# Kernel optimization log

Measured on AMD Instinct MI355X. Metric: run time of the kernel, lower is better.

The kernel has to match this reference:

```python
import jax, jax.numpy as jnp
import numpy as np

N_EMBD = 768
N_HEAD = 12
HEAD_DIM = N_EMBD // N_HEAD


def setup_inputs() -> dict:
    key = jax.random.key(0)
    ks = jax.random.split(key, 5)
    B, S = 4, 2048
    x = jax.random.normal(ks[0], (B, S, N_EMBD), dtype=jnp.float32)
    scale = 0.02
    w_attn = jax.random.normal(ks[1], (N_EMBD, 3 * N_EMBD), dtype=jnp.float32) * scale
    b_attn = jnp.zeros((3 * N_EMBD,), dtype=jnp.float32)
    w_proj = jax.random.normal(ks[2], (N_EMBD, N_EMBD), dtype=jnp.float32) * scale
    b_proj = jnp.zeros((N_EMBD,), dtype=jnp.float32)
    return {"x": x, "w_attn": w_attn, "b_attn": b_attn, "w_proj": w_proj, "b_proj": b_proj}


def reference(x, w_attn, b_attn, w_proj, b_proj):
    B, S, E = x.shape
    qkv = x @ w_attn + b_attn  # [B,S,3E]
    q, k, v = jnp.split(qkv, 3, axis=2)
    # [B,H,S,D]
    q = q.reshape(B, S, N_HEAD, HEAD_DIM).transpose(0, 2, 1, 3)
    k = k.reshape(B, S, N_HEAD, HEAD_DIM).transpose(0, 2, 1, 3)
    v = v.reshape(B, S, N_HEAD, HEAD_DIM).transpose(0, 2, 1, 3)
    scores = jnp.einsum('bhqd,bhkd->bhqk', q, k) / jnp.sqrt(jnp.float32(HEAD_DIM))
    causal = jnp.tril(jnp.ones((S, S), dtype=bool))
    scores = jnp.where(causal[None, None], scores, jnp.float32(-jnp.inf))
    weights = jax.nn.softmax(scores, axis=-1)
    out = jnp.einsum('bhqk,bhkd->bhqd', weights, v)
    out = out.transpose(0, 2, 1, 3).reshape(B, S, E)
    return out @ w_proj + b_proj
```

## Files before the change

kernel.cpp:

```cpp
#include <hip/hip_runtime.h>
#include <hip/hip_bf16.h>

typedef __attribute__((ext_vector_type(8))) __bf16 bf16x8;
typedef __attribute__((ext_vector_type(4))) __bf16 bf16x4;
typedef __attribute__((ext_vector_type(4))) float f32x4;

#define E_ 768
#define HEADS 12
#define HD 64
#define S_ 2048
#define B_ 4

__device__ inline unsigned short f2bf(float f) {
    union { float f; unsigned int u; } x{f};
    unsigned int r = x.u + 0x7FFFu + ((x.u >> 16) & 1u);
    return (unsigned short)(r >> 16);
}

__global__ void cvt_kernel(const float* __restrict__ in, unsigned short* __restrict__ out, int n4) {
    int i = blockIdx.x * blockDim.x + threadIdx.x;
    if (i < n4) {
        float4 v = reinterpret_cast<const float4*>(in)[i];
        ushort4 o;
        o.x = f2bf(v.x); o.y = f2bf(v.y); o.z = f2bf(v.z); o.w = f2bf(v.w);
        reinterpret_cast<ushort4*>(out)[i] = o;
    }
}

__global__ void transpose_cvt(const float* __restrict__ w, unsigned short* __restrict__ wT,
                              int K, int N) {
    __shared__ float tile[32][33];
    int n0 = blockIdx.x * 32, k0 = blockIdx.y * 32;
    int tx = threadIdx.x, ty = threadIdx.y;
    tile[ty][tx] = w[(size_t)(k0 + ty) * N + n0 + tx];
    __syncthreads();
    wT[(size_t)(n0 + ty) * K + k0 + tx] = f2bf(tile[tx][ty]);
}

template<int MODE>
__global__ __launch_bounds__(256) void gemm16(
    const unsigned short* __restrict__ A, const unsigned short* __restrict__ Bt,
    const float* __restrict__ bias,
    unsigned short* __restrict__ Qo, unsigned short* __restrict__ Ko,
    unsigned short* __restrict__ Vt, float* __restrict__ Of,
    int M, int N, int K)
{
    __shared__ unsigned short Sh[128 * 128];
    unsigned short* Ash = Sh;
    unsigned short* Bsh = Sh + 128 * 64;

    const int nbx = N >> 7;
    const int nwg = (M >> 7) * nbx;
    const int cpx = nwg >> 3;
    const int orig = blockIdx.x;
    const int wgid = (orig & 7) * cpx + (orig >> 3);
    const int row0 = (wgid / nbx) * 128;
    const int col0 = (wgid % nbx) * 128;

    const int t = threadIdx.x;
    const int w = t >> 6, lane = t & 63;
    const int lr = lane & 15, lc = lane >> 4;
    const int wrow = (w >> 1) * 64;
    const int wcol = (w & 1) * 64;

    const int srow = lane >> 3;
    const int sslot = lane & 7;

    f32x4 acc[4][4] = {};

    for (int k0 = 0; k0 < K; k0 += 64) {
#pragma unroll
        for (int j = 0; j < 4; j++) {
            const int rbase = j * 32 + w * 8;
            const unsigned short* ga = A + (size_t)(row0 + rbase + srow) * K + k0 + sslot * 8;
            __builtin_amdgcn_global_load_lds(
                (const __attribute__((address_space(1))) void*)ga,
                (__attribute__((address_space(3))) void*)&Ash[rbase * 64], 16, 0, 0);
            const unsigned short* gb = Bt + (size_t)(col0 + rbase + srow) * K + k0 + sslot * 8;
            __builtin_amdgcn_global_load_lds(
                (const __attribute__((address_space(1))) void*)gb,
                (__attribute__((address_space(3))) void*)&Bsh[rbase * 64], 16, 0, 0);
        }
        __syncthreads();

#pragma unroll
        for (int ks = 0; ks < 2; ks++) {
            bf16x8 a[4], b[4];
#pragma unroll
            for (int i = 0; i < 4; i++)
                a[i] = *reinterpret_cast<const bf16x8*>(&Ash[(wrow + i * 16 + lr) * 64 + ks * 32 + lc * 8]);
#pragma unroll
            for (int j2 = 0; j2 < 4; j2++)
                b[j2] = *reinterpret_cast<const bf16x8*>(&Bsh[(wcol + j2 * 16 + lr) * 64 + ks * 32 + lc * 8]);
#pragma unroll
            for (int i = 0; i < 4; i++)
#pragma unroll
                for (int j2 = 0; j2 < 4; j2++)
                    acc[i][j2] = __builtin_amdgcn_mfma_f32_16x16x32_bf16(a[i], b[j2], acc[i][j2], 0, 0, 0);
        }
        __syncthreads();
    }

    if constexpr (MODE == 0) {
        if (col0 >= 2 * E_) {
#pragma unroll
            for (int i = 0; i < 4; i++)
#pragma unroll
                for (int j = 0; j < 4; j++) {
                    const int c = wcol + j * 16 + lr;
                    const float bv = bias[col0 + c];
#pragma unroll
                    for (int r = 0; r < 4; r++) {
                        const int row = wrow + i * 16 + lc * 4 + r;
                        Sh[c * 128 + (row ^ ((c & 15) << 3))] = f2bf(acc[i][j][r] + bv);
                    }
                }
            __syncthreads();
            const int bb = row0 >> 11;
            const int s0 = row0 & (S_ - 1);
            const int nnb = col0 - 2 * E_;
#pragma unroll
            for (int pass = 0; pass < 8; pass++) {
                const int c = pass * 16 + (t >> 4);
                const int sL = (t & 15) * 8;
                bf16x8 vv = *reinterpret_cast<const bf16x8*>(&Sh[c * 128 + (sL ^ ((c & 15) << 3))]);
                const int h = (nnb + c) >> 6, d = c & 63;
                const size_t bh = (size_t)(bb * HEADS + h);
                *reinterpret_cast<bf16x8*>(&Vt[(bh * HD + d) * S_ + s0 + sL]) = vv;
            }
            return;
        }
#pragma unroll
        for (int i = 0; i < 4; i++)
#pragma unroll
            for (int j = 0; j < 4; j++) {
                int col = col0 + wcol + j * 16 + lr;
                float bv = bias[col];
#pragma unroll
                for (int r = 0; r < 4; r++) {
                    int row = row0 + wrow + i * 16 + lc * 4 + r;
                    float val = acc[i][j][r] + bv;
                    int bb = row >> 11, s = row & (S_ - 1);
                    int which = col / E_;
                    int nn = col - which * E_;
                    int h = nn >> 6, d = nn & 63;
                    size_t bh = (size_t)(bb * HEADS + h);
                    if (which == 0)      Qo[(bh * S_ + s) * HD + d] = f2bf(val * 0.125f);
                    else                 Ko[(bh * S_ + s) * HD + d] = f2bf(val);
                }
            }
    } else {
#pragma unroll
        for (int i = 0; i < 4; i++)
#pragma unroll
            for (int j = 0; j < 4; j++) {
                int col = col0 + wcol + j * 16 + lr;
                float bv = bias[col];
#pragma unroll
                for (int r = 0; r < 4; r++) {
                    int row = row0 + wrow + i * 16 + lc * 4 + r;
                    Of[(size_t)row * N + col] = acc[i][j][r] + bv;
                }
            }
    }
}

__global__ __launch_bounds__(256) void attn_kernel(
    const unsigned short* __restrict__ Q, const unsigned short* __restrict__ Kd,
    const unsigned short* __restrict__ Vt, unsigned short* __restrict__ O)
{
    __shared__ unsigned short Ksh[128 * 64];
    __shared__ unsigned short Vsh[64 * 128];
    __shared__ unsigned short Pl[4][16 * 128];

    const int t = threadIdx.x;
    const int w = t >> 6, lane = t & 63;
    const int lr = lane & 15, lc = lane >> 4;
    const int g = blockIdx.x;
    const int bp = g / 48;
    const int bh = g - bp * 48;
    const int tTL = bp, tTH = 31 - bp;
    const int qLrow0 = tTL * 64 + w * 16;
    const int qHrow0 = tTH * 64 + w * 16;
    const int nL = (tTL + 2) >> 1;

    const unsigned short* Qb = Q + (size_t)bh * S_ * HD;
    const unsigned short* Kb = Kd + (size_t)bh * S_ * HD;
    const unsigned short* Vb = Vt + (size_t)bh * HD * S_;

    const int srK = t >> 3, ssK = t & 7;
    const int kws = ((ssK ^ (srK & 7)) << 3);
    const int srV = t >> 4, ssV = t & 15;
    const int vws = ((ssV ^ (srV & 15)) << 3);
    const int r7 = lr & 7;

    const unsigned short* KbS = Kb + (size_t)srK * HD + ssK * 8;
    const unsigned short* VbS = Vb + (size_t)srV * S_ + ssV * 8;

    bf16x8 aqL[2], aqH[2];
#pragma unroll
    for (int dc = 0; dc < 2; dc++) {
        aqL[dc] = *reinterpret_cast<const bf16x8*>(Qb + (size_t)(qLrow0 + lr) * HD + dc * 32 + lc * 8);
        aqH[dc] = *reinterpret_cast<const bf16x8*>(Qb + (size_t)(qHrow0 + lr) * HD + dc * 32 + lc * 8);
    }

    f32x4 o[4] = {};
    float m = -INFINITY, l = 0.f;

    int bb = bh / HEADS, hh = bh - bb * HEADS;

    bf16x8 kreg[4], vreg[4];
#pragma unroll
    for (int i = 0; i < 4; i++) {
        kreg[i] = *reinterpret_cast<const bf16x8*>(KbS + i * 32 * HD);
        vreg[i] = *reinterpret_cast<const bf16x8*>(VbS + i * 16 * S_);
    }

    bf16x8 aq0 = aqL[0], aq1 = aqL[1];
    int qrow = qLrow0 + lr;

    for (int it = 0; it < 17; ++it) {
        __syncthreads();
#pragma unroll
        for (int i = 0; i < 4; i++) {
            *reinterpret_cast<bf16x8*>(&Ksh[(srK + i * 32) * 64 + kws]) = kreg[i];
            *reinterpret_cast<bf16x8*>(&Vsh[(srV + i * 16) * 128 + vws]) = vreg[i];
        }
        __syncthreads();

        if (it + 1 < 17) {
            const int nkv0 = (it + 1 < nL) ? (it + 1) * 128 : (it + 1 - nL) * 128;
#pragma unroll
            for (int i = 0; i < 4; i++) {
                kreg[i] = *reinterpret_cast<const bf16x8*>(KbS + (size_t)nkv0 * HD + i * 32 * HD);
                vreg[i] = *reinterpret_cast<const bf16x8*>(VbS + nkv0 + i * 16 * S_);
            }
        }

        if (it == nL) {
            float lq[4];
#pragma unroll
            for (int r = 0; r < 4; r++) lq[r] = __shfl(l, lc * 4 + r);
#pragma unroll
            for (int r = 0; r < 4; r++) {
                float inv = 1.f / lq[r];
                int qr = qLrow0 + lc * 4 + r;
#pragma unroll
                for (int dt = 0; dt < 4; dt++)
                    O[((size_t)(bb * S_ + qr)) * E_ + hh * HD + dt * 16 + lr] = f2bf(o[dt][r] * inv);
            }
            m = -INFINITY; l = 0.f;
#pragma unroll
            for (int dt = 0; dt < 4; dt++)
#pragma unroll
                for (int r = 0; r < 4; r++) o[dt][r] = 0.f;
            aq0 = aqH[0]; aq1 = aqH[1];
            qrow = qHrow0 + lr;
        }

        const int kv0 = (it < nL) ? it * 128 : (it - nL) * 128;
        const bool needMask = (it == nL - 1) || (it == 16);

        float p[8][4];
#pragma unroll
        for (int kt = 0; kt < 8; kt++) {
            const int row = kt * 16 + lr;
            const bf16x8 bk0 = *reinterpret_cast<const bf16x8*>(&Ksh[row * 64 + ((lc ^ r7) << 3)]);
            const bf16x8 bk1 = *reinterpret_cast<const bf16x8*>(&Ksh[row * 64 + (((4 + lc) ^ r7) << 3)]);
            f32x4 s = {};
            s = __builtin_amdgcn_mfma_f32_16x16x32_bf16(bk0, aq0, s, 0, 0, 0);
            s = __builtin_amdgcn_mfma_f32_16x16x32_bf16(bk1, aq1, s, 0, 0, 0);
#pragma unroll
            for (int r = 0; r < 4; r++) p[kt][r] = s[r];
        }
        if (needMask) {
#pragma unroll
            for (int kt = 0; kt < 8; kt++) {
                const int kbase = kv0 + kt * 16 + lc * 4;
#pragma unroll
                for (int r = 0; r < 4; r++)
                    if (kbase + r > qrow) p[kt][r] = -1e30f;
            }
        }

        float rm = -1e30f;
#pragma unroll
        for (int kt = 0; kt < 8; kt++)
#pragma unroll
            for (int r = 0; r < 4; r++) rm = fmaxf(rm, p[kt][r]);
        rm = fmaxf(rm, __shfl_xor(rm, 16));
        rm = fmaxf(rm, __shfl_xor(rm, 32));

        float mn = fmaxf(m, rm);
        float sc = __expf(m - mn);
        float rs = 0.f;
#pragma unroll
        for (int kt = 0; kt < 8; kt++)
#pragma unroll
            for (int r = 0; r < 4; r++) {
                float e = __expf(p[kt][r] - mn);
                p[kt][r] = e; rs += e;
            }
        rs += __shfl_xor(rs, 16);
        rs += __shfl_xor(rs, 32);
        l = l * sc + rs;
        m = mn;

        float scq[4];
#pragma unroll
        for (int r = 0; r < 4; r++) scq[r] = __shfl(sc, lc * 4 + r);
#pragma unroll
        for (int dt = 0; dt < 4; dt++)
#pragma unroll
            for (int r = 0; r < 4; r++) o[dt][r] *= scq[r];

#pragma unroll
        for (int kt = 0; kt < 8; kt++) {
            bf16x4 pv4;
            pv4[0] = (__bf16)p[kt][0]; pv4[1] = (__bf16)p[kt][1];
            pv4[2] = (__bf16)p[kt][2]; pv4[3] = (__bf16)p[kt][3];
            const int phys = (2 * kt + (lc >> 1)) ^ r7;
            *reinterpret_cast<bf16x4*>(&Pl[w][lr * 128 + phys * 8 + (lc & 1) * 4]) = pv4;
        }
        asm volatile("s_waitcnt lgkmcnt(0)" ::: "memory");
        __builtin_amdgcn_sched_barrier(0);

        bf16x8 ap[4];
#pragma unroll
        for (int kc = 0; kc < 4; kc++)
            ap[kc] = *reinterpret_cast<const bf16x8*>(&Pl[w][lr * 128 + (((kc * 4 + lc) ^ r7) << 3)]);

#pragma unroll
        for (int dt = 0; dt < 4; dt++) {
            const int row = dt * 16 + lr;
#pragma unroll
            for (int kc = 0; kc < 4; kc++) {
                const bf16x8 bv = *reinterpret_cast<const bf16x8*>(
                    &Vsh[row * 128 + (((kc * 4 + lc) ^ lr) << 3)]);
                o[dt] = __builtin_amdgcn_mfma_f32_16x16x32_bf16(ap[kc], bv, o[dt], 0, 0, 0);
            }
        }
    }

    {
        float lq[4];
#pragma unroll
        for (int r = 0; r < 4; r++) lq[r] = __shfl(l, lc * 4 + r);
#pragma unroll
        for (int r = 0; r < 4; r++) {
            float inv = 1.f / lq[r];
            int qr = qHrow0 + lc * 4 + r;
#pragma unroll
            for (int dt = 0; dt < 4; dt++)
                O[((size_t)(bb * S_ + qr)) * E_ + hh * HD + dt * 16 + lr] = f2bf(o[dt][r] * inv);
        }
    }
}

extern "C" void kernel_launch(void* const* d_in, const int* in_sizes, int n_in,
                              void* d_out, int out_size, void* d_ws, size_t ws_size,
                              hipStream_t stream) {
    const float* x      = (const float*)d_in[0];
    const float* w_attn = (const float*)d_in[1];
    const float* b_attn = (const float*)d_in[2];
    const float* w_proj = (const float*)d_in[3];
    const float* b_proj = (const float*)d_in[4];
    float* out = (float*)d_out;

    char* ws = (char*)d_ws;
    const size_t M = (size_t)B_ * S_;
    unsigned short* xb  = (unsigned short*)(ws);
    unsigned short* waT = (unsigned short*)(ws + 12582912);
    unsigned short* wpT = (unsigned short*)(ws + 16121856);
    unsigned short* Qb  = (unsigned short*)(ws + 17301504);
    unsigned short* Kb  = (unsigned short*)(ws + 29884416);
    unsigned short* Vt  = (unsigned short*)(ws + 42467328);
    unsigned short* AO  = (unsigned short*)(ws + 55050240);

    int n4 = (int)(M * E_ / 4);
    cvt_kernel<<<(n4 + 255) / 256, 256, 0, stream>>>(x, xb, n4);
    transpose_cvt<<<dim3(3 * E_ / 32, E_ / 32), dim3(32, 32), 0, stream>>>(w_attn, waT, E_, 3 * E_);
    transpose_cvt<<<dim3(E_ / 32, E_ / 32), dim3(32, 32), 0, stream>>>(w_proj, wpT, E_, E_);

    gemm16<0><<<1152, 256, 0, stream>>>(
        xb, waT, b_attn, Qb, Kb, Vt, nullptr, (int)M, 3 * E_, E_);

    attn_kernel<<<768, 256, 0, stream>>>(Qb, Kb, Vt, AO);

    gemm16<1><<<384, 256, 0, stream>>>(
        AO, wpT, b_proj, nullptr, nullptr, nullptr, out, (int)M, E_, E_);
}
```

Baseline: 167.0 us.

## Feed P to PV MFMA from registers, permute V reads to match

Drops the per-wave LDS round trip for the softmax probabilities. P is now packed directly from the QK MFMA accumulator registers into the A operand of the PV MFMA, and V fragments are gathered from shared memory with two 8-byte loads in a permuted k-order that matches the register layout. This removes LDS writes, a wait, and LDS reads per iteration, at the cost of narrower V loads. It also raises wave priority around the MFMA blocks with s_setprio.

```diff
diff --git a/kernel.cpp b/kernel.cpp
--- a/kernel.cpp
+++ b/kernel.cpp
@@ -4,6 +4,7 @@
 typedef __attribute__((ext_vector_type(8))) __bf16 bf16x8;
 typedef __attribute__((ext_vector_type(4))) __bf16 bf16x4;
 typedef __attribute__((ext_vector_type(4))) float f32x4;
+typedef __attribute__((ext_vector_type(2))) unsigned int u32x2;
 
 #define E_ 768
 #define HEADS 12
@@ -171,7 +172,6 @@
 {
     __shared__ unsigned short Ksh[128 * 64];
     __shared__ unsigned short Vsh[64 * 128];
-    __shared__ unsigned short Pl[4][16 * 128];
 
     const int t = threadIdx.x;
     const int w = t >> 6, lane = t & 63;
@@ -262,6 +262,7 @@
         const bool needMask = (it == nL - 1) || (it == 16);
 
         float p[8][4];
+        __builtin_amdgcn_s_setprio(1);
 #pragma unroll
         for (int kt = 0; kt < 8; kt++) {
             const int row = kt * 16 + lr;
@@ -273,6 +274,7 @@
 #pragma unroll
             for (int r = 0; r < 4; r++) p[kt][r] = s[r];
         }
+        __builtin_amdgcn_s_setprio(0);
         if (needMask) {
 #pragma unroll
             for (int kt = 0; kt < 8; kt++) {
@@ -314,32 +316,34 @@
 #pragma unroll
             for (int r = 0; r < 4; r++) o[dt][r] *= scq[r];
 
-#pragma unroll
-        for (int kt = 0; kt < 8; kt++) {
-            bf16x4 pv4;
-            pv4[0] = (__bf16)p[kt][0]; pv4[1] = (__bf16)p[kt][1];
-            pv4[2] = (__bf16)p[kt][2]; pv4[3] = (__bf16)p[kt][3];
-            const int phys = (2 * kt + (lc >> 1)) ^ r7;
-            *reinterpret_cast<bf16x4*>(&Pl[w][lr * 128 + phys * 8 + (lc & 1) * 4]) = pv4;
-        }
-        asm volatile("s_waitcnt lgkmcnt(0)" ::: "memory");
-        __builtin_amdgcn_sched_barrier(0);
-
         bf16x8 ap[4];
 #pragma unroll
-        for (int kc = 0; kc < 4; kc++)
-            ap[kc] = *reinterpret_cast<const bf16x8*>(&Pl[w][lr * 128 + (((kc * 4 + lc) ^ r7) << 3)]);
-
+        for (int kc = 0; kc < 4; kc++) {
+            union { bf16x8 v; __bf16 b[8]; } u;
+            u.b[0] = (__bf16)p[2 * kc][0];     u.b[1] = (__bf16)p[2 * kc][1];
+            u.b[2] = (__bf16)p[2 * kc][2];     u.b[3] = (__bf16)p[2 * kc][3];
+            u.b[4] = (__bf16)p[2 * kc + 1][0]; u.b[5] = (__bf16)p[2 * kc + 1][1];
+            u.b[6] = (__bf16)p[2 * kc + 1][2]; u.b[7] = (__bf16)p[2 * kc + 1][3];
+            ap[kc] = u.v;
+        }
+
+        __builtin_amdgcn_s_setprio(1);
 #pragma unroll
         for (int dt = 0; dt < 4; dt++) {
             const int row = dt * 16 + lr;
+            const int m15 = row & 15;
+            const int half = (lc & 1) * 4;
 #pragma unroll
             for (int kc = 0; kc < 4; kc++) {
-                const bf16x8 bv = *reinterpret_cast<const bf16x8*>(
-                    &Vsh[row * 128 + (((kc * 4 + lc) ^ lr) << 3)]);
-                o[dt] = __builtin_amdgcn_mfma_f32_16x16x32_bf16(ap[kc], bv, o[dt], 0, 0, 0);
-            }
-        }
+                union { bf16x8 v; u32x2 h[2]; } bu;
+                bu.h[0] = *reinterpret_cast<const u32x2*>(
+                    &Vsh[row * 128 + (((kc * 4 + (lc >> 1)) ^ m15) << 3) + half]);
+                bu.h[1] = *reinterpret_cast<const u32x2*>(
+                    &Vsh[row * 128 + (((kc * 4 + 2 + (lc >> 1)) ^ m15) << 3) + half]);
+                o[dt] = __builtin_amdgcn_mfma_f32_16x16x32_bf16(ap[kc], bu.v, o[dt], 0, 0, 0);
+            }
+        }
+        __builtin_amdgcn_s_setprio(0);
     }
 
     {
```

After: 173.0 us. 1.04x slower.
